# Kernel optimization log

Hardware: AMD Instinct MI355X
Metric: run time of the kernel (lower is better)

## Reference

```python
import jax, jax.numpy as jnp
import numpy as np

THRESHOLD = 1.0

def setup_inputs() -> dict:
    key = jax.random.key(0)
    k1, k2 = jax.random.split(key)
    us_alphas = jax.random.uniform(k1, (4096, 8192), dtype=jnp.float32)
    integrate = jax.random.uniform(k2, (4096,), dtype=jnp.float32)
    return {"us_alphas": us_alphas, "integrate": integrate}

def reference(us_alphas, integrate):
    # us_alphas: [B, T], integrate: [B]
    # CIF without hidden: accumulate alpha per step, record pre-reset value,
    # subtract threshold wherever the accumulator fired.
    def step(acc, alpha_t):
        acc = acc + alpha_t                                  # [B]
        fire = acc                                           # recorded BEFORE reset
        acc = jnp.where(acc >= THRESHOLD, acc - THRESHOLD, acc)
        return acc, fire

    integrate_new, fires_tb = jax.lax.scan(step, integrate, us_alphas.T)
    fires = fires_tb.T                                        # [B, T]
    return fires, integrate_new
```

## Files before the change

kernel.cpp:

```cpp
#include <hip/hip_runtime.h>


constexpr int Bn   = 4096;
constexpr int Tn   = 8192;
constexpr int R    = 8;
constexpr int C    = 256;
constexpr int S    = R + 1;
constexpr int NIT  = Tn / C;
constexpr int NBLK = Bn / R;

__device__ __forceinline__ float cif_fract(float s){
#if __has_builtin(__builtin_amdgcn_fractf)
    return __builtin_amdgcn_fractf(s);
#else
    return s - floorf(s);
#endif
}

__global__ __launch_bounds__(256)
void cif_fused(const float* __restrict__ A,
               const float* __restrict__ integ,
               float* __restrict__ fires,
               float* __restrict__ out_int)
{
    __shared__ float lds[2][C][S];
    const int tid     = threadIdx.x;
    const int rowbase = blockIdx.x * R;

    const int r   = (tid >> 3) & (R - 1);
    const int c4a = (tid & 7) + 8 * (tid >> 6);
    const int c4b = c4a + 32;

    const float4* __restrict__ src = (const float4*)A + (size_t)(rowbase + r) * (Tn / 4);
    float4* __restrict__       dst = (float4*)fires   + (size_t)(rowbase + r) * (Tn / 4);

    auto write_tile = [&](int bf, const float4& a, const float4& b){
        const int ca = 4 * c4a, cb = 4 * c4b;
        lds[bf][ca + 0][r] = a.x;
        lds[bf][ca + 1][r] = a.y;
        lds[bf][ca + 2][r] = a.z;
        lds[bf][ca + 3][r] = a.w;
        lds[bf][cb + 0][r] = b.x;
        lds[bf][cb + 1][r] = b.y;
        lds[bf][cb + 2][r] = b.z;
        lds[bf][cb + 3][r] = b.w;
    };

    {
        float4 a = src[c4a];
        float4 b = src[c4b];
        write_tile(0, a, b);
    }
    float acc = (tid < R) ? integ[rowbase + tid] : 0.f;
    __syncthreads();

    for (int it = 0; it < NIT; ++it){
        const int bf = it & 1;

        float4 pa, pb;
        const bool pf = (it + 1 < NIT);
        if (pf){
            pa = src[(it + 1) * (C / 4) + c4a];
            pb = src[(it + 1) * (C / 4) + c4b];
        }

        if (tid < R){
            #pragma unroll
            for (int c = 0; c < C; ++c){
                float s = acc + lds[bf][c][tid];
                lds[bf][c][tid] = s;
                acc = cif_fract(s);
            }
        }
        __syncthreads();

        {
            const int ca = 4 * c4a, cb = 4 * c4b;
            float4 w0, w1;
            w0.x = lds[bf][ca + 0][r]; w0.y = lds[bf][ca + 1][r];
            w0.z = lds[bf][ca + 2][r]; w0.w = lds[bf][ca + 3][r];
            w1.x = lds[bf][cb + 0][r]; w1.y = lds[bf][cb + 1][r];
            w1.z = lds[bf][cb + 2][r]; w1.w = lds[bf][cb + 3][r];
            dst[it * (C / 4) + c4a] = w0;
            dst[it * (C / 4) + c4b] = w1;
        }

        if (pf)
            write_tile(bf ^ 1, pa, pb);

        __syncthreads();
    }

    if (tid < R) out_int[rowbase + tid] = acc;
}

extern "C" void kernel_launch(void* const* d_in, const int* in_sizes, int n_in,
                              void* d_out, int out_size, void* d_ws, size_t ws_size,
                              hipStream_t stream)
{
    const float* A     = (const float*)d_in[0];
    const float* integ = (const float*)d_in[1];
    float* out = (float*)d_out;

    hipLaunchKernelGGL(cif_fused, dim3(NBLK), dim3(256), 0, stream,
                       A, integ, out, out + (size_t)Bn * Tn);
}
```

Measured before the change: 300.4 us.

## Warp-specialize CIF scan with triple-buffered LDS and row-major float4 tiles

Splits each block into one compute wavefront that runs the sequential scan and four wavefronts that load and store, using a three-slot LDS ring. Compute of tile k now overlaps the writeback of tile k-1 and the prefetch of tile k+1, with one barrier per tile instead of two. The LDS layout changes to row-major with padding so the scan thread reads and writes float4s. Rows per block double to 16 and the tile width halves to 128, which halves the block count. The serial chain is still one lane per row, and 16 active lanes in one wave may leave most of the wavefront idle.

```diff
diff --git a/kernel.cpp b/kernel.cpp
--- a/kernel.cpp
+++ b/kernel.cpp
@@ -3,11 +3,12 @@
 
 constexpr int Bn   = 4096;
 constexpr int Tn   = 8192;
-constexpr int R    = 8;
-constexpr int C    = 256;
-constexpr int S    = R + 1;
-constexpr int NIT  = Tn / C;
+constexpr int R    = 16;
+constexpr int C    = 128;
+constexpr int LSTR = C + 4;
+constexpr int NT   = Tn / C;
 constexpr int NBLK = Bn / R;
+constexpr int NTHR = 320;
 
 __device__ __forceinline__ float cif_fract(float s){
 #if __has_builtin(__builtin_amdgcn_fractf)
@@ -17,80 +18,79 @@
 #endif
 }
 
-__global__ __launch_bounds__(256)
+__global__ __launch_bounds__(NTHR)
 void cif_fused(const float* __restrict__ A,
                const float* __restrict__ integ,
                float* __restrict__ fires,
                float* __restrict__ out_int)
 {
-    __shared__ float lds[2][C][S];
+    __shared__ float lds[3][R][LSTR];
     const int tid     = threadIdx.x;
     const int rowbase = blockIdx.x * R;
 
-    const int r   = (tid >> 3) & (R - 1);
-    const int c4a = (tid & 7) + 8 * (tid >> 6);
-    const int c4b = c4a + 32;
+    const bool is_comp = (tid < 64);
 
-    const float4* __restrict__ src = (const float4*)A + (size_t)(rowbase + r) * (Tn / 4);
-    float4* __restrict__       dst = (float4*)fires   + (size_t)(rowbase + r) * (Tn / 4);
+    const int sid = tid - 64;
+    const int r0  = (sid >> 5) & 7;
+    const int r1  = r0 + 8;
+    const int c4  = sid & 31;
 
-    auto write_tile = [&](int bf, const float4& a, const float4& b){
-        const int ca = 4 * c4a, cb = 4 * c4b;
-        lds[bf][ca + 0][r] = a.x;
-        lds[bf][ca + 1][r] = a.y;
-        lds[bf][ca + 2][r] = a.z;
-        lds[bf][ca + 3][r] = a.w;
-        lds[bf][cb + 0][r] = b.x;
-        lds[bf][cb + 1][r] = b.y;
-        lds[bf][cb + 2][r] = b.z;
-        lds[bf][cb + 3][r] = b.w;
-    };
+    const float4* __restrict__ srcf4 = (const float4*)A;
+    float4*       __restrict__ dstf4 = (float4*)fires;
+    const size_t rowstr = Tn / 4;
 
-    {
-        float4 a = src[c4a];
-        float4 b = src[c4b];
-        write_tile(0, a, b);
+    if (!is_comp){
+        float4 a0 = srcf4[(size_t)(rowbase + r0) * rowstr + c4];
+        float4 a1 = srcf4[(size_t)(rowbase + r1) * rowstr + c4];
+        *(float4*)&lds[0][r0][4 * c4] = a0;
+        *(float4*)&lds[0][r1][4 * c4] = a1;
     }
     float acc = (tid < R) ? integ[rowbase + tid] : 0.f;
     __syncthreads();
 
-    for (int it = 0; it < NIT; ++it){
-        const int bf = it & 1;
+    int cur = 0;
+    for (int k = 0; k < NT; ++k){
+        const int nxt = (cur == 2) ? 0 : cur + 1;
+        const int prv = (cur == 0) ? 2 : cur - 1;
 
-        float4 pa, pb;
-        const bool pf = (it + 1 < NIT);
-        if (pf){
-            pa = src[(it + 1) * (C / 4) + c4a];
-            pb = src[(it + 1) * (C / 4) + c4b];
-        }
-
-        if (tid < R){
-            #pragma unroll
-            for (int c = 0; c < C; ++c){
-                float s = acc + lds[bf][c][tid];
-                lds[bf][c][tid] = s;
-                acc = cif_fract(s);
+        if (is_comp){
+            if (tid < R){
+                float4* rowp = (float4*)&lds[cur][tid][0];
+                #pragma unroll
+                for (int g = 0; g < C / 4; ++g){
+                    float4 v = rowp[g];
+                    float s0 = acc + v.x; acc = cif_fract(s0);
+                    float s1 = acc + v.y; acc = cif_fract(s1);
+                    float s2 = acc + v.z; acc = cif_fract(s2);
+                    float s3 = acc + v.w; acc = cif_fract(s3);
+                    rowp[g] = make_float4(s0, s1, s2, s3);
+                }
+            }
+        } else {
+            if (k > 0){
+                float4 f0 = *(const float4*)&lds[prv][r0][4 * c4];
+                float4 f1 = *(const float4*)&lds[prv][r1][4 * c4];
+                dstf4[(size_t)(rowbase + r0) * rowstr + (size_t)(k - 1) * (C / 4) + c4] = f0;
+                dstf4[(size_t)(rowbase + r1) * rowstr + (size_t)(k - 1) * (C / 4) + c4] = f1;
+            }
+            if (k + 1 < NT){
+                float4 a0 = srcf4[(size_t)(rowbase + r0) * rowstr + (size_t)(k + 1) * (C / 4) + c4];
+                float4 a1 = srcf4[(size_t)(rowbase + r1) * rowstr + (size_t)(k + 1) * (C / 4) + c4];
+                *(float4*)&lds[nxt][r0][4 * c4] = a0;
+                *(float4*)&lds[nxt][r1][4 * c4] = a1;
             }
         }
         __syncthreads();
-
-        {
-            const int ca = 4 * c4a, cb = 4 * c4b;
-            float4 w0, w1;
-            w0.x = lds[bf][ca + 0][r]; w0.y = lds[bf][ca + 1][r];
-            w0.z = lds[bf][ca + 2][r]; w0.w = lds[bf][ca + 3][r];
-            w1.x = lds[bf][cb + 0][r]; w1.y = lds[bf][cb + 1][r];
-            w1.z = lds[bf][cb + 2][r]; w1.w = lds[bf][cb + 3][r];
-            dst[it * (C / 4) + c4a] = w0;
-            dst[it * (C / 4) + c4b] = w1;
-        }
-
-        if (pf)
-            write_tile(bf ^ 1, pa, pb);
-
-        __syncthreads();
+        cur = nxt;
     }
 
+    if (!is_comp){
+        const int prv = (cur == 0) ? 2 : cur - 1;
+        float4 f0 = *(const float4*)&lds[prv][r0][4 * c4];
+        float4 f1 = *(const float4*)&lds[prv][r1][4 * c4];
+        dstf4[(size_t)(rowbase + r0) * rowstr + (size_t)(NT - 1) * (C / 4) + c4] = f0;
+        dstf4[(size_t)(rowbase + r1) * rowstr + (size_t)(NT - 1) * (C / 4) + c4] = f1;
+    }
     if (tid < R) out_int[rowbase + tid] = acc;
 }
 
@@ -102,6 +102,6 @@
     const float* integ = (const float*)d_in[1];
     float* out = (float*)d_out;
 
-    hipLaunchKernelGGL(cif_fused, dim3(NBLK), dim3(256), 0, stream,
+    hipLaunchKernelGGL(cif_fused, dim3(NBLK), dim3(NTHR), 0, stream,
                        A, integ, out, out + (size_t)Bn * Tn);
 }
```

Measured after the change: 251.4 us. 1.19x faster.
